# Kernel optimization log

Hardware: AMD Instinct MI355X
Metric: run time of the kernel (lower is better)

The kernel has to match this reference:

```python
import jax, jax.numpy as jnp
import numpy as np

B, S, D = 8, 2048, 512
H, LAT, OUT = 8, 64, 64


def setup_inputs() -> dict:
    key = jax.random.key(0)
    ks = jax.random.split(key, 5)
    return {
        "x": jax.random.normal(ks[0], (B, S, D), dtype=jnp.float32),
        "WQ": jax.random.normal(ks[1], (H, D, LAT), dtype=jnp.float32) * 0.05,
        "WK": jax.random.normal(ks[2], (H, D, LAT), dtype=jnp.float32) * 0.05,
        "WV": jax.random.normal(ks[3], (H, D, OUT), dtype=jnp.float32) * 0.05,
        "WO": jax.random.normal(ks[4], (H * OUT, OUT), dtype=jnp.float32) * 0.05,
    }


def reference(x, WQ, WK, WV, WO):
    # Per-head projections, vectorized over heads (faithful to the TF python loop).
    Q = jnp.einsum('bsd,hdk->bhsk', x, WQ)   # [B,H,S,LAT]
    K = jnp.einsum('bsd,hdk->bhsk', x, WK)   # [B,H,S,LAT]
    V = jnp.einsum('bsd,hdo->bhso', x, WV)   # [B,H,S,OUT]
    scale = jnp.asarray(1.0 / np.sqrt(LAT), dtype=x.dtype)
    A = jnp.einsum('bhqk,bhsk->bhqs', Q, K) * scale  # [B,H,S,S]
    A = jax.nn.softmax(A, axis=-1)
    O = jnp.einsum('bhqs,bhso->bhqo', A, V)  # [B,H,S,OUT]
    # concat heads along last axis (head 0 first, matching the TF loop order)
    O = jnp.transpose(O, (0, 2, 1, 3)).reshape(x.shape[0], x.shape[1], H * OUT)
    return O @ WO  # [B,S,OUT]
```

## Files before the change

### kernel.cpp

```cpp
#include <hip/hip_runtime.h>
#include <hip/hip_bf16.h>
#include <math.h>

static constexpr int Bn = 8, Sn = 2048, Dn = 512, Hn = 8, LATn = 64, OUTn = 64;

typedef short  bf16x8 __attribute__((ext_vector_type(8)));
typedef float  f32x4  __attribute__((ext_vector_type(4)));

__device__ __forceinline__ unsigned short f2bf(float f) {
    union { float f; unsigned int i; } v; v.f = f;
    unsigned int x = v.i;
    return (unsigned short)((x + 0x7FFFu + ((x >> 16) & 1u)) >> 16);
}
__device__ __forceinline__ unsigned int pack2bf(float a, float b) {
    unsigned int ua = __float_as_uint(a) + 0x8000u;
    unsigned int ub = __float_as_uint(b) + 0x8000u;
    return (ua >> 16) | (ub & 0xFFFF0000u);
}

#if __has_builtin(__builtin_amdgcn_exp2f)
#define EXP2(x) __builtin_amdgcn_exp2f(x)
#else
#define EXP2(x) exp2f(x)
#endif

__device__ __forceinline__ void gl_lds16(const void* g, void* l) {
    __builtin_amdgcn_global_load_lds(
        (const __attribute__((address_space(1))) unsigned int*)g,
        (__attribute__((address_space(3))) unsigned int*)l, 16, 0, 0);
}

__global__ __launch_bounds__(256) void wprep(
    const float* __restrict__ WQ, const float* __restrict__ WK,
    const float* __restrict__ WV, const float* __restrict__ WO,
    unsigned short* __restrict__ WT)
{
    __shared__ float tile[64][65];
    const int t  = threadIdx.x;
    const int d0 = blockIdx.x * 64;
    const int yy = blockIdx.y;

    const float* W; float scale = 1.0f; size_t dstbase;
    if (yy < 24) {
        int h = yy / 3, which = yy % 3;
        W = (which == 0) ? WQ : (which == 1) ? WK : WV;
        W += (size_t)h * Dn * 64;
        if (which == 0) scale = 0.125f * 1.44269504088896f;
        dstbase = ((size_t)h * 192 + which * 64) * Dn;
    } else {
        W = WO;
        dstbase = (size_t)8 * 192 * Dn;
    }

    for (int i = 0; i < 4; ++i) {
        int idx = i * 256 + t;
        int r = idx >> 4, c = (idx & 15) * 4;
        float4 u = *(const float4*)(W + (size_t)(d0 + r) * 64 + c);
        tile[r][c] = u.x; tile[r][c+1] = u.y; tile[r][c+2] = u.z; tile[r][c+3] = u.w;
    }
    __syncthreads();
    const int n = t & 63, dd = t >> 6;
    unsigned short pk[16];
    for (int i = 0; i < 16; ++i) pk[i] = f2bf(tile[dd*16 + i][n] * scale);
    size_t dst = dstbase + (size_t)n * Dn + d0 + dd * 16;
    *(bf16x8*)(WT + dst)     = *(bf16x8*)(pk);
    *(bf16x8*)(WT + dst + 8) = *(bf16x8*)(pk + 8);
}

__global__ __launch_bounds__(256) void qkv_mfma(
    const float* __restrict__ x, const unsigned short* __restrict__ WT,
    unsigned short* __restrict__ Qb, unsigned short* __restrict__ Kb,
    unsigned short* __restrict__ VT)
{
    __shared__ __align__(16) unsigned short lds[64*72 + 192*72];
    unsigned short* Xs = lds;
    unsigned short* Ws = lds + 64*72;
    unsigned short* L  = lds;

    const int t  = threadIdx.x;
    const int w  = t >> 6, ln = t & 63;
    const int nl = ln & 15, g = ln >> 4;
    const int bh = blockIdx.y, b = bh >> 3, h = bh & 7;
    const int s0 = blockIdx.x * 64;

    f32x4 acc[4][3];
    for (int m = 0; m < 4; ++m)
        for (int j = 0; j < 3; ++j) acc[m][j] = (f32x4){0.f, 0.f, 0.f, 0.f};

    for (int k0 = 0; k0 < Dn; k0 += 64) {
        __syncthreads();
        for (int i = 0; i < 2; ++i) {
            int idx = i * 256 + t;
            int r = idx >> 3, c = (idx & 7) * 8;
            const float* src = x + ((size_t)(b * Sn + s0 + r)) * Dn + k0 + c;
            float4 u0 = *(const float4*)(src);
            float4 u1 = *(const float4*)(src + 4);
            unsigned int pk[4] = { pack2bf(u0.x, u0.y), pack2bf(u0.z, u0.w),
                                   pack2bf(u1.x, u1.y), pack2bf(u1.z, u1.w) };
            *(bf16x8*)(Xs + r*72 + c) = *(bf16x8*)pk;
        }
        for (int i = 0; i < 6; ++i) {
            int idx = i * 256 + t;
            int r = idx >> 3, c = (idx & 7) * 8;
            *(bf16x8*)(Ws + r*72 + c) =
                *(const bf16x8*)(WT + ((size_t)h * 192 + r) * Dn + k0 + c);
        }
        __syncthreads();
        #pragma unroll
        for (int kc = 0; kc < 2; ++kc) {
            bf16x8 a[4], bb[3];
            for (int m = 0; m < 4; ++m)
                a[m]  = *(const bf16x8*)(Xs + (16*m + nl)*72 + 32*kc + 8*g);
            for (int j = 0; j < 3; ++j)
                bb[j] = *(const bf16x8*)(Ws + ((3*w + j)*16 + nl)*72 + 32*kc + 8*g);
            for (int m = 0; m < 4; ++m)
                for (int j = 0; j < 3; ++j)
                    acc[m][j] = __builtin_amdgcn_mfma_f32_16x16x32_bf16(
                                    a[m], bb[j], acc[m][j], 0, 0, 0);
        }
    }
    __syncthreads();
    for (int m = 0; m < 4; ++m)
        for (int j = 0; j < 3; ++j) {
            int n = 48*w + 16*j + nl;
            for (int r = 0; r < 4; ++r)
                L[(16*m + 4*g + r)*200 + n] = f2bf(acc[m][j][r]);
        }
    __syncthreads();
    for (int i = 0; i < 4; ++i) {
        int idx = i * 256 + t;
        int r = idx >> 4, c = (idx & 15) * 8;
        bf16x8 v = *(const bf16x8*)(L + r*200 + c);
        size_t o = ((size_t)bh * Sn + s0 + r) * 64;
        if (c < 64) *(bf16x8*)(Qb + o + c)      = v;
        else        *(bf16x8*)(Kb + o + c - 64) = v;
    }
    {
        int o = t & 63, cc = t >> 6;
        unsigned short pk[16];
        for (int i = 0; i < 16; ++i) pk[i] = L[(16*cc + i)*200 + 128 + o];
        size_t dst = ((size_t)bh * 64 + o) * Sn + s0 + 16*cc;
        *(bf16x8*)(VT + dst)     = *(bf16x8*)(pk);
        *(bf16x8*)(VT + dst + 8) = *(bf16x8*)(pk + 8);
    }
}

__global__ __launch_bounds__(512, 4) void flash_mfma(
    const unsigned short* __restrict__ Qb,
    const unsigned short* __restrict__ Kb,
    const unsigned short* __restrict__ VT,
    unsigned short* __restrict__ Ob)
{
    __shared__ __align__(16) unsigned short KV[2][2][4096];
    __shared__ __align__(16) unsigned short Pt[8][2048];

    const int t  = threadIdx.x;
    const int w  = t >> 6, ln = t & 63;
    const int qh = ln & 15, g = (ln >> 4) & 3;
    const int bh = blockIdx.y, b = bh >> 3, h = bh & 7;
    const int q0 = blockIdx.x * 256;
    const int qw = q0 + 32 * w;

    bf16x8 bq[2][2];
    #pragma unroll
    for (int qs = 0; qs < 2; ++qs) {
        const unsigned short* qp =
            Qb + ((size_t)bh * Sn + qw + 16*qs + qh) * 64 + 8*g;
        bq[qs][0] = *(const bf16x8*)(qp);
        bq[qs][1] = *(const bf16x8*)(qp + 32);
    }

    const int r0 = t >> 3;
    const int cs = (t & 7) ^ (r0 & 7);
    const unsigned short* kg = Kb + ((size_t)bh * Sn + r0) * 64 + cs * 8;
    const unsigned short* vg = VT + ((size_t)bh * 64 + r0) * Sn + cs * 8;

    const int swz8  = (qh & 7) * 8;
    const int koff0 = qh*64 + (((g    ) ^ (qh & 7)) * 8);
    const int koff1 = qh*64 + (((4 + g) ^ (qh & 7)) * 8);

    f32x4 o_acc[2][4];
    #pragma unroll
    for (int qs = 0; qs < 2; ++qs)
        #pragma unroll
        for (int f = 0; f < 4; ++f) o_acc[qs][f] = (f32x4){0.f, 0.f, 0.f, 0.f};
    float l_run[2] = {0.f, 0.f};

    gl_lds16(kg, &KV[0][0][w * 512]);
    gl_lds16(vg, &KV[0][1][w * 512]);
    __syncthreads();

    int buf = 0;
    for (int kt = 0; kt < Sn / 64; ++kt) {
        if (kt < Sn / 64 - 1) {
            kg += 4096; vg += 64;
            gl_lds16(kg, &KV[buf ^ 1][0][w * 512]);
            gl_lds16(vg, &KV[buf ^ 1][1][w * 512]);
        }
        const unsigned short* Kt = KV[buf][0];
        const unsigned short* Vt = KV[buf][1];

        f32x4 st[2][4];
        #pragma unroll
        for (int qs = 0; qs < 2; ++qs)
            #pragma unroll
            for (int f = 0; f < 4; ++f) st[qs][f] = (f32x4){0.f, 0.f, 0.f, 0.f};
        #pragma unroll
        for (int kc = 0; kc < 2; ++kc) {
            const int ko = kc ? koff1 : koff0;
            bf16x8 a0 = *(const bf16x8*)(Kt + ko);
            bf16x8 a1 = *(const bf16x8*)(Kt + ko + 1024);
            bf16x8 a2 = *(const bf16x8*)(Kt + ko + 2048);
            bf16x8 a3 = *(const bf16x8*)(Kt + ko + 3072);
            #pragma unroll
            for (int qs = 0; qs < 2; ++qs) {
                st[qs][0] = __builtin_amdgcn_mfma_f32_16x16x32_bf16(a0, bq[qs][kc], st[qs][0], 0, 0, 0);
                st[qs][1] = __builtin_amdgcn_mfma_f32_16x16x32_bf16(a1, bq[qs][kc], st[qs][1], 0, 0, 0);
                st[qs][2] = __builtin_amdgcn_mfma_f32_16x16x32_bf16(a2, bq[qs][kc], st[qs][2], 0, 0, 0);
                st[qs][3] = __builtin_amdgcn_mfma_f32_16x16x32_bf16(a3, bq[qs][kc], st[qs][3], 0, 0, 0);
            }
        }

        #pragma unroll
        for (int qs = 0; qs < 2; ++qs) {
            float ls = 0.f;
            unsigned short* pw = Pt[w] + qs*1024 + qh*64;
            #pragma unroll
            for (int f = 0; f < 4; ++f) {
                float p0 = EXP2(st[qs][f][0]);
                float p1 = EXP2(st[qs][f][1]);
                float p2 = EXP2(st[qs][f][2]);
                float p3 = EXP2(st[qs][f][3]);
                ls += (p0 + p1) + (p2 + p3);
                *(uint2*)(pw + ((16*f + 4*g) ^ swz8)) =
                    make_uint2(pack2bf(p0, p1), pack2bf(p2, p3));
            }
            ls += __shfl_xor(ls, 16);
            ls += __shfl_xor(ls, 32);
            l_run[qs] += ls;
        }

        #pragma unroll
        for (int kc = 0; kc < 2; ++kc) {
            const int ko = kc ? koff1 : koff0;
            bf16x8 v0 = *(const bf16x8*)(Vt + ko);
            bf16x8 v1 = *(const bf16x8*)(Vt + ko + 1024);
            bf16x8 v2 = *(const bf16x8*)(Vt + ko + 2048);
            bf16x8 v3 = *(const bf16x8*)(Vt + ko + 3072);
            #pragma unroll
            for (int qs = 0; qs < 2; ++qs) {
                bf16x8 bp = *(const bf16x8*)(Pt[w] + qs*1024 + qh*64
                                             + ((32*kc + 8*g) ^ swz8));
                o_acc[qs][0] = __builtin_amdgcn_mfma_f32_16x16x32_bf16(v0, bp, o_acc[qs][0], 0, 0, 0);
                o_acc[qs][1] = __builtin_amdgcn_mfma_f32_16x16x32_bf16(v1, bp, o_acc[qs][1], 0, 0, 0);
                o_acc[qs][2] = __builtin_amdgcn_mfma_f32_16x16x32_bf16(v2, bp, o_acc[qs][2], 0, 0, 0);
                o_acc[qs][3] = __builtin_amdgcn_mfma_f32_16x16x32_bf16(v3, bp, o_acc[qs][3], 0, 0, 0);
            }
        }

        __syncthreads();
        buf ^= 1;
    }

    #pragma unroll
    for (int qs = 0; qs < 2; ++qs) {
        float inv_l = 1.f / l_run[qs];
        unsigned short* op = Ob
            + ((size_t)(b * Sn + q0 + 32*w + 16*qs + qh)) * 512 + h*64 + 4*g;
        #pragma unroll
        for (int f = 0; f < 4; ++f) {
            unsigned int lo = pack2bf(o_acc[qs][f][0] * inv_l, o_acc[qs][f][1] * inv_l);
            unsigned int hi = pack2bf(o_acc[qs][f][2] * inv_l, o_acc[qs][f][3] * inv_l);
            *(uint2*)(op + 16*f) = make_uint2(lo, hi);
        }
    }
}

__global__ __launch_bounds__(256) void out_mfma(
    const unsigned short* __restrict__ Ob, const unsigned short* __restrict__ WOT,
    float* __restrict__ out)
{
    __shared__ __align__(16) unsigned short As[64 * 72];
    __shared__ __align__(16) unsigned short Bs[64 * 72];

    const int t  = threadIdx.x;
    const int w  = t >> 6, ln = t & 63;
    const int qh = ln & 15, g = ln >> 4;
    const int bs0 = blockIdx.x * 64;

    f32x4 acc[4];
    for (int n = 0; n < 4; ++n) acc[n] = (f32x4){0.f, 0.f, 0.f, 0.f};

    for (int k0 = 0; k0 < 512; k0 += 64) {
        __syncthreads();
        for (int i = 0; i < 2; ++i) {
            int idx = i * 256 + t;
            int r = idx >> 3, c = (idx & 7) * 8;
            *(bf16x8*)(As + r*72 + c) =
                *(const bf16x8*)(Ob + ((size_t)(bs0 + r)) * 512 + k0 + c);
            *(bf16x8*)(Bs + r*72 + c) =
                *(const bf16x8*)(WOT + (size_t)r * Dn + k0 + c);
        }
        __syncthreads();
        #pragma unroll
        for (int kc = 0; kc < 2; ++kc) {
            bf16x8 a = *(const bf16x8*)(As + (16*w + qh)*72 + 32*kc + 8*g);
            #pragma unroll
            for (int n = 0; n < 4; ++n) {
                bf16x8 bb = *(const bf16x8*)(Bs + (16*n + qh)*72 + 32*kc + 8*g);
                acc[n] = __builtin_amdgcn_mfma_f32_16x16x32_bf16(a, bb, acc[n], 0, 0, 0);
            }
        }
    }
    for (int n = 0; n < 4; ++n)
        for (int r = 0; r < 4; ++r)
            out[((size_t)(bs0 + 16*w + 4*g + r)) * 64 + 16*n + qh] = acc[n][r];
}

extern "C" void kernel_launch(void* const* d_in, const int* in_sizes, int n_in,
                              void* d_out, int out_size, void* d_ws, size_t ws_size,
                              hipStream_t stream)
{
    const float* x  = (const float*)d_in[0];
    const float* WQ = (const float*)d_in[1];
    const float* WK = (const float*)d_in[2];
    const float* WV = (const float*)d_in[3];
    const float* WO = (const float*)d_in[4];
    float* out = (float*)d_out;

    const size_t NQ = (size_t)Bn * Hn * Sn * LATn;
    char* p = (char*)d_ws;
    unsigned short* Qb  = (unsigned short*)p;           p += NQ * 2;
    unsigned short* Kb  = (unsigned short*)p;           p += NQ * 2;
    unsigned short* VT  = (unsigned short*)p;           p += NQ * 2;
    unsigned short* WT  = (unsigned short*)p;           p += ((size_t)Hn*192*Dn + 64*Dn) * 2;
    unsigned short* Ob  = (unsigned short*)p;
    unsigned short* WOT = WT + (size_t)Hn * 192 * Dn;

    wprep     <<<dim3(8, 25),         256, 0, stream>>>(WQ, WK, WV, WO, WT);
    qkv_mfma  <<<dim3(Sn/64, Bn*Hn),  256, 0, stream>>>(x, WT, Qb, Kb, VT);
    flash_mfma<<<dim3(Sn/256, Bn*Hn), 512, 0, stream>>>(Qb, Kb, VT, Ob);
    out_mfma  <<<dim3(Bn*Sn/64),      256, 0, stream>>>(Ob, WOT, out);
}
```

Before: 221.1 us.

## Reuse staged x tile across all heads in QKV projection with double-buffered weights

The QKV projection kernel now assigns one block per (batch, 64-row) tile. The block converts x to bf16 once into a full-width swizzled LDS tile and loops over all 8 heads, streaming weight slices through a double-buffered LDS pipeline with asynchronous global-to-LDS loads. This removes the 8x redundant reading and conversion of x from global memory. In exchange the grid has 8x fewer, larger blocks that use much more LDS, which lowers occupancy and parallelism.

Result: slower. 234.7 us (+6.1%).

```diff
diff --git a/kernel.cpp b/kernel.cpp
--- a/kernel.cpp
+++ b/kernel.cpp
@@ -67,81 +67,109 @@
     *(bf16x8*)(WT + dst + 8) = *(bf16x8*)(pk + 8);
 }
 
-__global__ __launch_bounds__(256) void qkv_mfma(
+__global__ __launch_bounds__(512, 2) void qkv_mfma(
     const float* __restrict__ x, const unsigned short* __restrict__ WT,
     unsigned short* __restrict__ Qb, unsigned short* __restrict__ Kb,
     unsigned short* __restrict__ VT)
 {
-    __shared__ __align__(16) unsigned short lds[64*72 + 192*72];
-    unsigned short* Xs = lds;
-    unsigned short* Ws = lds + 64*72;
-    unsigned short* L  = lds;
+    __shared__ __align__(16) unsigned short Xs[64 * 512];
+    __shared__ __align__(16) unsigned short Ws[2][192 * 64];
+    __shared__ __align__(16) unsigned short Os[64 * 200];
 
     const int t  = threadIdx.x;
     const int w  = t >> 6, ln = t & 63;
     const int nl = ln & 15, g = ln >> 4;
-    const int bh = blockIdx.y, b = bh >> 3, h = bh & 7;
+    const int b  = blockIdx.y;
     const int s0 = blockIdx.x * 64;
-
-    f32x4 acc[4][3];
-    for (int m = 0; m < 4; ++m)
-        for (int j = 0; j < 3; ++j) acc[m][j] = (f32x4){0.f, 0.f, 0.f, 0.f};
-
-    for (int k0 = 0; k0 < Dn; k0 += 64) {
+    const int wm = w >> 2;
+    const int wn = w & 3;
+
+    #pragma unroll
+    for (int i = 0; i < 8; ++i) {
+        const int r = 8 * i + w;
+        const float* src = x + ((size_t)b * Sn + s0 + r) * Dn + 8 * ln;
+        float4 u0 = *(const float4*)(src);
+        float4 u1 = *(const float4*)(src + 4);
+        unsigned int pk[4] = { pack2bf(u0.x, u0.y), pack2bf(u0.z, u0.w),
+                               pack2bf(u1.x, u1.y), pack2bf(u1.z, u1.w) };
+        *(bf16x8*)(Xs + r * 512 + ((ln ^ w) * 8)) = *(bf16x8*)pk;
+    }
+
+    const int nbase = w * 8 + (ln >> 3);
+    const int csw   = ((ln & 7) ^ (ln >> 3)) * 8;
+    auto stageW = [&](int h, int k0, int bufi) {
+        #pragma unroll
+        for (int i = 0; i < 3; ++i) {
+            const int n = i * 64 + nbase;
+            gl_lds16(WT + ((size_t)h * 192 + n) * Dn + k0 + csw,
+                     Ws[bufi] + (size_t)i * 4096 + w * 512);
+        }
+    };
+
+    stageW(0, 0, 0);
+    __syncthreads();
+
+    int buf = 0;
+    for (int h = 0; h < Hn; ++h) {
+        f32x4 acc[2][3];
+        #pragma unroll
+        for (int m = 0; m < 2; ++m)
+            #pragma unroll
+            for (int j = 0; j < 3; ++j) acc[m][j] = (f32x4){0.f, 0.f, 0.f, 0.f};
+
+        for (int ks = 0; ks < 8; ++ks) {
+            int nh = h, nks = ks + 1;
+            if (nks == 8) { nks = 0; ++nh; }
+            if (nh < Hn) stageW(nh, nks * 64, buf ^ 1);
+
+            const unsigned short* Wb = Ws[buf];
+            const int k0 = ks * 64;
+            #pragma unroll
+            for (int kc = 0; kc < 2; ++kc) {
+                const int sc = ((4 * kc + g) ^ (nl & 7)) * 8;
+                bf16x8 a0 = *(const bf16x8*)(Xs + (32*wm      + nl) * 512 + k0 + sc);
+                bf16x8 a1 = *(const bf16x8*)(Xs + (32*wm + 16 + nl) * 512 + k0 + sc);
+                bf16x8 b0 = *(const bf16x8*)(Wb + (48*wn      + nl) * 64 + sc);
+                bf16x8 b1 = *(const bf16x8*)(Wb + (48*wn + 16 + nl) * 64 + sc);
+                bf16x8 b2 = *(const bf16x8*)(Wb + (48*wn + 32 + nl) * 64 + sc);
+                acc[0][0] = __builtin_amdgcn_mfma_f32_16x16x32_bf16(a0, b0, acc[0][0], 0, 0, 0);
+                acc[0][1] = __builtin_amdgcn_mfma_f32_16x16x32_bf16(a0, b1, acc[0][1], 0, 0, 0);
+                acc[0][2] = __builtin_amdgcn_mfma_f32_16x16x32_bf16(a0, b2, acc[0][2], 0, 0, 0);
+                acc[1][0] = __builtin_amdgcn_mfma_f32_16x16x32_bf16(a1, b0, acc[1][0], 0, 0, 0);
+                acc[1][1] = __builtin_amdgcn_mfma_f32_16x16x32_bf16(a1, b1, acc[1][1], 0, 0, 0);
+                acc[1][2] = __builtin_amdgcn_mfma_f32_16x16x32_bf16(a1, b2, acc[1][2], 0, 0, 0);
+            }
+            __syncthreads();
+            buf ^= 1;
+        }
+
+        const int bh = b * 8 + h;
+        #pragma unroll
+        for (int m = 0; m < 2; ++m)
+            #pragma unroll
+            for (int j = 0; j < 3; ++j) {
+                const int n = 48 * wn + 16 * j + nl;
+                #pragma unroll
+                for (int r = 0; r < 4; ++r)
+                    Os[(32*wm + 16*m + 4*g + r) * 200 + n] = f2bf(acc[m][j][r]);
+            }
         __syncthreads();
         for (int i = 0; i < 2; ++i) {
-            int idx = i * 256 + t;
-            int r = idx >> 3, c = (idx & 7) * 8;
-            const float* src = x + ((size_t)(b * Sn + s0 + r)) * Dn + k0 + c;
-            float4 u0 = *(const float4*)(src);
-            float4 u1 = *(const float4*)(src + 4);
-            unsigned int pk[4] = { pack2bf(u0.x, u0.y), pack2bf(u0.z, u0.w),
-                                   pack2bf(u1.x, u1.y), pack2bf(u1.z, u1.w) };
-            *(bf16x8*)(Xs + r*72 + c) = *(bf16x8*)pk;
-        }
-        for (int i = 0; i < 6; ++i) {
-            int idx = i * 256 + t;
-            int r = idx >> 3, c = (idx & 7) * 8;
-            *(bf16x8*)(Ws + r*72 + c) =
-                *(const bf16x8*)(WT + ((size_t)h * 192 + r) * Dn + k0 + c);
-        }
-        __syncthreads();
-        #pragma unroll
-        for (int kc = 0; kc < 2; ++kc) {
-            bf16x8 a[4], bb[3];
-            for (int m = 0; m < 4; ++m)
-                a[m]  = *(const bf16x8*)(Xs + (16*m + nl)*72 + 32*kc + 8*g);
-            for (int j = 0; j < 3; ++j)
-                bb[j] = *(const bf16x8*)(Ws + ((3*w + j)*16 + nl)*72 + 32*kc + 8*g);
-            for (int m = 0; m < 4; ++m)
-                for (int j = 0; j < 3; ++j)
-                    acc[m][j] = __builtin_amdgcn_mfma_f32_16x16x32_bf16(
-                                    a[m], bb[j], acc[m][j], 0, 0, 0);
-        }
-    }
-    __syncthreads();
-    for (int m = 0; m < 4; ++m)
-        for (int j = 0; j < 3; ++j) {
-            int n = 48*w + 16*j + nl;
-            for (int r = 0; r < 4; ++r)
-                L[(16*m + 4*g + r)*200 + n] = f2bf(acc[m][j][r]);
-        }
-    __syncthreads();
-    for (int i = 0; i < 4; ++i) {
-        int idx = i * 256 + t;
-        int r = idx >> 4, c = (idx & 15) * 8;
-        bf16x8 v = *(const bf16x8*)(L + r*200 + c);
-        size_t o = ((size_t)bh * Sn + s0 + r) * 64;
-        if (c < 64) *(bf16x8*)(Qb + o + c)      = v;
-        else        *(bf16x8*)(Kb + o + c - 64) = v;
-    }
-    {
-        int o = t & 63, cc = t >> 6;
-        unsigned short pk[16];
-        for (int i = 0; i < 16; ++i) pk[i] = L[(16*cc + i)*200 + 128 + o];
-        size_t dst = ((size_t)bh * 64 + o) * Sn + s0 + 16*cc;
-        *(bf16x8*)(VT + dst)     = *(bf16x8*)(pk);
-        *(bf16x8*)(VT + dst + 8) = *(bf16x8*)(pk + 8);
+            int idx = i * 512 + t;
+            int r = idx >> 4, c = (idx & 15) * 8;
+            bf16x8 v = *(const bf16x8*)(Os + r * 200 + c);
+            size_t o = ((size_t)bh * Sn + s0 + r) * 64;
+            if (c < 64) *(bf16x8*)(Qb + o + c)      = v;
+            else        *(bf16x8*)(Kb + o + c - 64) = v;
+        }
+        {
+            int o = t & 63, cc = t >> 6;
+            unsigned short pk[8];
+            #pragma unroll
+            for (int i = 0; i < 8; ++i) pk[i] = Os[(8*cc + i) * 200 + 128 + o];
+            *(bf16x8*)(VT + ((size_t)bh * 64 + o) * Sn + s0 + 8*cc) = *(bf16x8*)pk;
+        }
+        __syncthreads();
     }
 }
 
@@ -338,7 +366,7 @@
     unsigned short* WOT = WT + (size_t)Hn * 192 * Dn;
 
     wprep     <<<dim3(8, 25),         256, 0, stream>>>(WQ, WK, WV, WO, WT);
-    qkv_mfma  <<<dim3(Sn/64, Bn*Hn),  256, 0, stream>>>(x, WT, Qb, Kb, VT);
+    qkv_mfma  <<<dim3(Sn/64, Bn),     512, 0, stream>>>(x, WT, Qb, Kb, VT);
     flash_mfma<<<dim3(Sn/256, Bn*Hn), 512, 0, stream>>>(Qb, Kb, VT, Ob);
     out_mfma  <<<dim3(Bn*Sn/64),      256, 0, stream>>>(Ob, WOT, out);
 }
```
